# Optimization experiments

Measured on AMD Instinct MI355X. Metric: run time of the kernel, lower is better.

The kernel has to match this reference:

```python
import jax, jax.numpy as jnp
import numpy as np

B, L, H = 4, 512, 768
S, R = 100, 100          # num spans, num relations
E = 25                   # size embedding dim
MAXLEN = 100             # max entity length (size embedding vocab)
NE, NR = 10, 6           # entity / relation type counts
NEG = jnp.float32(-1e20)


def _span_masks(key, batch, n, seqlen, max_len):
    k1, k2 = jax.random.split(key)
    starts = jax.random.randint(k1, (batch, n), 0, seqlen - max_len)
    lens = jax.random.randint(k2, (batch, n), 1, max_len)
    pos = jnp.arange(seqlen)
    m = (pos[None, None, :] >= starts[..., None]) & (pos[None, None, :] < (starts + lens)[..., None])
    return m.astype(jnp.int32)  # (batch, n, seqlen), contiguous 0/1 spans


def setup_inputs() -> dict:
    key = jax.random.key(0)
    ks = jax.random.split(key, 8)
    hidden_states = jax.random.normal(ks[0], (B, L, H), dtype=jnp.float32)
    entity_masks = _span_masks(ks[1], B, S, L, 20)            # span len < MAXLEN
    relation_context_masks = _span_masks(ks[2], B, R, L, 50)  # context len < MAXLEN
    relations = jax.random.randint(ks[3], (B, R, 2), 0, S)
    size_emb = jax.random.normal(ks[4], (MAXLEN, E), dtype=jnp.float32) * 0.02
    w_span = jax.random.normal(ks[5], (E + H, NE), dtype=jnp.float32) * 0.02
    b_span = jnp.zeros((NE,), dtype=jnp.float32)
    w_rel = jax.random.normal(ks[6], (2 * E + 3 * H, NR), dtype=jnp.float32) * 0.02
    b_rel = jnp.zeros((NR,), dtype=jnp.float32)
    return {
        'hidden_states': hidden_states,
        'entity_masks': entity_masks,
        'relations': relations,
        'relation_context_masks': relation_context_masks,
        'size_emb': size_emb,
        'w_span': w_span,
        'b_span': b_span,
        'w_rel': w_rel,
        'b_rel': b_rel,
    }


def _masked_max(hidden, masks):
    # hidden: (B, L, H); masks: (B, N, L) 0/1 -> (B, N, H) max over masked positions
    # Matches torch: h.unsqueeze(1)*m then masked_fill(m==0, -1e20), max over L
    masked = jnp.where(masks[..., None] != 0, hidden[:, None, :, :], NEG)
    return jnp.max(masked, axis=-2)


def reference(hidden_states, entity_masks, relations, relation_context_masks,
              size_emb, w_span, b_span, w_rel, b_rel):
    # entity sizes -> size embedding lookup
    entity_sizes = size_emb[entity_masks.sum(-1)]                     # (B, S, E)

    # entity span max-pool + classify
    entities = _masked_max(hidden_states, entity_masks)               # (B, S, H)
    entity_reprs = jnp.concatenate([entities, entity_sizes], axis=-1)
    entity_logits = entity_reprs @ w_span + b_span                    # (B, S, NE)

    # relation context max-pool
    rel_ctx = _masked_max(hidden_states, relation_context_masks)      # (B, R, H)

    # gather entity pairs
    b, r = relations.shape[:2]
    rel_flat = relations.reshape(b, -1)                               # (B, 2R)
    pairs = jnp.take_along_axis(entities, rel_flat[:, :, None], axis=1).reshape(b, r, -1)
    pair_sizes = jnp.take_along_axis(entity_sizes, rel_flat[:, :, None], axis=1).reshape(b, r, -1)

    rel_reprs = jnp.concatenate([rel_ctx, pairs, pair_sizes], axis=-1)
    relation_logits = rel_reprs @ w_rel + b_rel                       # (B, R, NR)
    return entity_logits, relation_logits
```

## Files before the change

### kernel.cpp

```cpp
#include <hip/hip_runtime.h>

#define B 4
#define L 512
#define H 768
#define S 100
#define R 100
#define E 25
#define NE 10
#define NR 6
#define NEGF (-1e20f)
#define TPB 192

__device__ __forceinline__ float4 fmax4(float4 a, float4 b) {
    return make_float4(fmaxf(a.x, b.x), fmaxf(a.y, b.y),
                       fmaxf(a.z, b.z), fmaxf(a.w, b.w));
}

__device__ __forceinline__ void mask_stats(const int* __restrict__ mrow,
                                           int t, int wave, int lane,
                                           int* sc, int* sm, int& n, int& start)
{
    int4 m = make_int4(0, 0, 0, 0);
    if (t < L / 4) m = reinterpret_cast<const int4*>(mrow)[t];
    const unsigned long long b0 = __ballot(m.x != 0);
    const unsigned long long b1 = __ballot(m.y != 0);
    const unsigned long long b2 = __ballot(m.z != 0);
    const unsigned long long b3 = __ballot(m.w != 0);
    if (lane == 0 && wave < 2) {
        const int c = __popcll(b0) + __popcll(b1) + __popcll(b2) + __popcll(b3);
        int mn = L;
        if (b3) mn = min(mn, 4 * __builtin_ctzll(b3) + 3);
        if (b2) mn = min(mn, 4 * __builtin_ctzll(b2) + 2);
        if (b1) mn = min(mn, 4 * __builtin_ctzll(b1) + 1);
        if (b0) mn = min(mn, 4 * __builtin_ctzll(b0));
        sc[wave] = c;
        sm[wave] = (mn < L) ? (256 * wave + mn) : L;
    }
    __syncthreads();
    n = sc[0] + sc[1];
    start = min(sm[0], sm[1]);
}

__device__ __forceinline__ float4 span_pool4(const float* __restrict__ hb,
                                             int start, int n, int t)
{
    const int st = H / 4;
    const float4* base = reinterpret_cast<const float4*>(hb) + (size_t)start * st + t;
    float4 a0 = make_float4(NEGF, NEGF, NEGF, NEGF);
    float4 a1 = a0, a2 = a0, a3 = a0, a4 = a0, a5 = a0, a6 = a0, a7 = a0;
    const int last = n - 1;
    for (int i = 0; i < n; i += 8) {
        const float4 v0 = base[(size_t)min(i + 0, last) * st];
        const float4 v1 = base[(size_t)min(i + 1, last) * st];
        const float4 v2 = base[(size_t)min(i + 2, last) * st];
        const float4 v3 = base[(size_t)min(i + 3, last) * st];
        const float4 v4 = base[(size_t)min(i + 4, last) * st];
        const float4 v5 = base[(size_t)min(i + 5, last) * st];
        const float4 v6 = base[(size_t)min(i + 6, last) * st];
        const float4 v7 = base[(size_t)min(i + 7, last) * st];
        a0 = fmax4(a0, v0); a1 = fmax4(a1, v1);
        a2 = fmax4(a2, v2); a3 = fmax4(a3, v3);
        a4 = fmax4(a4, v4); a5 = fmax4(a5, v5);
        a6 = fmax4(a6, v6); a7 = fmax4(a7, v7);
    }
    return fmax4(fmax4(fmax4(a0, a1), fmax4(a2, a3)),
                 fmax4(fmax4(a4, a5), fmax4(a6, a7)));
}

template <int NO>
__device__ __forceinline__ void block_reduce_store(float* p, int t, int wave, int lane,
                                                   float (*sred)[NO],
                                                   const float* __restrict__ bias,
                                                   float* __restrict__ outrow)
{
    #pragma unroll
    for (int o = 0; o < NO; ++o) {
        float v = p[o];
        for (int off = 32; off > 0; off >>= 1) v += __shfl_down(v, off, 64);
        p[o] = v;
    }
    if (lane == 0) {
        #pragma unroll
        for (int o = 0; o < NO; ++o) sred[wave][o] = p[o];
    }
    __syncthreads();
    if (t < NO) outrow[t] = sred[0][t] + sred[1][t] + sred[2][t] + bias[t];
}

__global__ __launch_bounds__(TPB) void pool_kernel(
    const float* __restrict__ hidden,
    const int*   __restrict__ emask,
    const int*   __restrict__ cmask,
    const float* __restrict__ size_emb,
    const float* __restrict__ w_span,
    const float* __restrict__ b_span,
    float* __restrict__ entities,
    int*   __restrict__ n_ent,
    float* __restrict__ rel_ctx,
    float* __restrict__ ent_logits)
{
    const int idx  = blockIdx.x;
    const int b    = idx / (S + R);
    const int j    = idx % (S + R);
    const int t    = threadIdx.x;
    const int wave = t >> 6;
    const int lane = t & 63;

    __shared__ int   sc[2], sm[2];
    __shared__ float sred[3][NE];

    const float* hb = hidden + (size_t)b * L * H;
    const int* mrow = (j < S) ? (emask + (size_t)(b * S + j) * L)
                              : (cmask + (size_t)(b * R + (j - S)) * L);
    int n, start;
    mask_stats(mrow, t, wave, lane, sc, sm, n, start);

    const float4 mv = span_pool4(hb, start, n, t);

    if (j >= S) {
        reinterpret_cast<float4*>(rel_ctx + (size_t)(b * R + (j - S)) * H)[t] = mv;
        return;
    }

    reinterpret_cast<float4*>(entities + (size_t)(b * S + j) * H)[t] = mv;
    if (t == 0) n_ent[b * S + j] = n;

    float p[NE];
    const float* w0 = w_span + (size_t)(4 * t) * NE;
    #pragma unroll
    for (int o = 0; o < NE; ++o)
        p[o] = mv.x * w0[o] + mv.y * w0[NE + o] + mv.z * w0[2 * NE + o] + mv.w * w0[3 * NE + o];
    if (t < E) {
        const float sz = size_emb[(size_t)n * E + t];
        #pragma unroll
        for (int o = 0; o < NE; ++o) p[o] += sz * w_span[(size_t)(H + t) * NE + o];
    }
    block_reduce_store<NE>(p, t, wave, lane, sred, b_span,
                           ent_logits + (size_t)(b * S + j) * NE);
}

__global__ __launch_bounds__(TPB) void rel_kernel(
    const float* __restrict__ entities,
    const int*   __restrict__ n_ent,
    const float* __restrict__ rel_ctx,
    const int*   __restrict__ relations,
    const float* __restrict__ size_emb,
    const float* __restrict__ w_rel,
    const float* __restrict__ b_rel,
    float* __restrict__ rel_logits)
{
    const int idx  = blockIdx.x;
    const int b    = idx / R;
    const int r    = idx % R;
    const int t    = threadIdx.x;
    const int wave = t >> 6;
    const int lane = t & 63;

    const int head = relations[(size_t)(b * R + r) * 2 + 0];
    const int tail = relations[(size_t)(b * R + r) * 2 + 1];

    const float4 c4 = reinterpret_cast<const float4*>(rel_ctx  + (size_t)(b * R + r)    * H)[t];
    const float4 h4 = reinterpret_cast<const float4*>(entities + (size_t)(b * S + head) * H)[t];
    const float4 t4 = reinterpret_cast<const float4*>(entities + (size_t)(b * S + tail) * H)[t];

    float p[NR];
    const float* wc = w_rel + (size_t)(4 * t) * NR;
    const float* wh = w_rel + (size_t)(H + 4 * t) * NR;
    const float* wt = w_rel + (size_t)(2 * H + 4 * t) * NR;
    #pragma unroll
    for (int o = 0; o < NR; ++o)
        p[o] = c4.x * wc[o] + c4.y * wc[NR + o] + c4.z * wc[2 * NR + o] + c4.w * wc[3 * NR + o]
             + h4.x * wh[o] + h4.y * wh[NR + o] + h4.z * wh[2 * NR + o] + h4.w * wh[3 * NR + o]
             + t4.x * wt[o] + t4.y * wt[NR + o] + t4.z * wt[2 * NR + o] + t4.w * wt[3 * NR + o];

    if (t < E) {
        const float sz = size_emb[(size_t)n_ent[b * S + head] * E + t];
        #pragma unroll
        for (int o = 0; o < NR; ++o) p[o] += sz * w_rel[(size_t)(3 * H + t) * NR + o];
    } else if (t >= 64 && t < 64 + E) {
        const int e = t - 64;
        const float sz = size_emb[(size_t)n_ent[b * S + tail] * E + e];
        #pragma unroll
        for (int o = 0; o < NR; ++o) p[o] += sz * w_rel[(size_t)(3 * H + E + e) * NR + o];
    }

    __shared__ float sred[3][NR];
    block_reduce_store<NR>(p, t, wave, lane, sred, b_rel,
                           rel_logits + (size_t)(b * R + r) * NR);
}

extern "C" void kernel_launch(void* const* d_in, const int* in_sizes, int n_in,
                              void* d_out, int out_size, void* d_ws, size_t ws_size,
                              hipStream_t stream) {
    const float* hidden    = (const float*)d_in[0];
    const int*   emask     = (const int*)  d_in[1];
    const int*   relations = (const int*)  d_in[2];
    const int*   cmask     = (const int*)  d_in[3];
    const float* size_emb  = (const float*)d_in[4];
    const float* w_span    = (const float*)d_in[5];
    const float* b_span    = (const float*)d_in[6];
    const float* w_rel     = (const float*)d_in[7];
    const float* b_rel     = (const float*)d_in[8];

    float* out        = (float*)d_out;
    float* ent_logits = out;
    float* rel_logits = out + B * S * NE;

    float* ws       = (float*)d_ws;
    float* entities = ws;
    float* rel_ctx  = entities + (size_t)B * S * H;
    int*   n_ent    = (int*)(rel_ctx + (size_t)B * R * H);

    pool_kernel<<<B * (S + R), TPB, 0, stream>>>(
        hidden, emask, cmask, size_emb, w_span, b_span,
        entities, n_ent, rel_ctx, ent_logits);

    rel_kernel<<<B * R, TPB, 0, stream>>>(
        entities, n_ent, rel_ctx, relations, size_emb, w_rel, b_rel, rel_logits);
}
```

Before: 84.79 us.

## Project entities to relation logits before gathering, replacing full-vector gather kernel

Uses the linearity of the relation classifier: each entity's pooled vector and size embedding are projected onto the head and tail halves of w_rel inside the pooling kernel, and each context vector is projected onto its part of w_rel there too. A small combine kernel then gathers and adds those 6-wide projections per relation. This removes writing and re-reading the full 768-wide entity and context vectors through the workspace, and replaces the second block-per-relation kernel with a cheap elementwise one. In exchange, the entity blocks do more reductions (22 outputs instead of 10), and floating-point summation order changes.

```diff
diff --git a/kernel.cpp b/kernel.cpp
--- a/kernel.cpp
+++ b/kernel.cpp
@@ -10,6 +10,7 @@
 #define NR 6
 #define NEGF (-1e20f)
 #define TPB 192
+#define NPROJ (NE + 2*NR)
 
 __device__ __forceinline__ float4 fmax4(float4 a, float4 b) {
     return make_float4(fmaxf(a.x, b.x), fmaxf(a.y, b.y),
@@ -68,23 +69,18 @@
 }
 
 template <int NO>
-__device__ __forceinline__ void block_reduce_store(float* p, int t, int wave, int lane,
-                                                   float (*sred)[NO],
-                                                   const float* __restrict__ bias,
-                                                   float* __restrict__ outrow)
+__device__ __forceinline__ float block_reduce(const float* p, int t, int wave, int lane,
+                                              float sred[3][NPROJ])
 {
     #pragma unroll
     for (int o = 0; o < NO; ++o) {
         float v = p[o];
+        #pragma unroll
         for (int off = 32; off > 0; off >>= 1) v += __shfl_down(v, off, 64);
-        p[o] = v;
-    }
-    if (lane == 0) {
-        #pragma unroll
-        for (int o = 0; o < NO; ++o) sred[wave][o] = p[o];
+        if (lane == 0) sred[wave][o] = v;
     }
     __syncthreads();
-    if (t < NO) outrow[t] = sred[0][t] + sred[1][t] + sred[2][t] + bias[t];
+    return (t < NO) ? (sred[0][t] + sred[1][t] + sred[2][t]) : 0.0f;
 }
 
 __global__ __launch_bounds__(TPB) void pool_kernel(
@@ -94,9 +90,10 @@
     const float* __restrict__ size_emb,
     const float* __restrict__ w_span,
     const float* __restrict__ b_span,
-    float* __restrict__ entities,
-    int*   __restrict__ n_ent,
-    float* __restrict__ rel_ctx,
+    const float* __restrict__ w_rel,
+    const float* __restrict__ b_rel,
+    float* __restrict__ ent_proj,
+    float* __restrict__ ctx_proj,
     float* __restrict__ ent_logits)
 {
     const int idx  = blockIdx.x;
@@ -107,7 +104,7 @@
     const int lane = t & 63;
 
     __shared__ int   sc[2], sm[2];
-    __shared__ float sred[3][NE];
+    __shared__ float sred[3][NPROJ];
 
     const float* hb = hidden + (size_t)b * L * H;
     const int* mrow = (j < S) ? (emask + (size_t)(b * S + j) * L)
@@ -118,75 +115,67 @@
     const float4 mv = span_pool4(hb, start, n, t);
 
     if (j >= S) {
-        reinterpret_cast<float4*>(rel_ctx + (size_t)(b * R + (j - S)) * H)[t] = mv;
+        float p[NR];
+        const float* wc = w_rel + (size_t)(4 * t) * NR;
+        #pragma unroll
+        for (int o = 0; o < NR; ++o)
+            p[o] = mv.x * wc[o] + mv.y * wc[NR + o]
+                 + mv.z * wc[2 * NR + o] + mv.w * wc[3 * NR + o];
+        const float r = block_reduce<NR>(p, t, wave, lane, sred);
+        if (t < NR)
+            ctx_proj[(size_t)(b * R + (j - S)) * NR + t] = r + b_rel[t];
         return;
     }
 
-    reinterpret_cast<float4*>(entities + (size_t)(b * S + j) * H)[t] = mv;
-    if (t == 0) n_ent[b * S + j] = n;
-
-    float p[NE];
+    float p[NPROJ];
     const float* w0 = w_span + (size_t)(4 * t) * NE;
+    const float* wh = w_rel  + (size_t)(H + 4 * t) * NR;
+    const float* wt = w_rel  + (size_t)(2 * H + 4 * t) * NR;
     #pragma unroll
     for (int o = 0; o < NE; ++o)
-        p[o] = mv.x * w0[o] + mv.y * w0[NE + o] + mv.z * w0[2 * NE + o] + mv.w * w0[3 * NE + o];
+        p[o] = mv.x * w0[o] + mv.y * w0[NE + o]
+             + mv.z * w0[2 * NE + o] + mv.w * w0[3 * NE + o];
+    #pragma unroll
+    for (int o = 0; o < NR; ++o) {
+        p[NE + o]      = mv.x * wh[o] + mv.y * wh[NR + o]
+                       + mv.z * wh[2 * NR + o] + mv.w * wh[3 * NR + o];
+        p[NE + NR + o] = mv.x * wt[o] + mv.y * wt[NR + o]
+                       + mv.z * wt[2 * NR + o] + mv.w * wt[3 * NR + o];
+    }
     if (t < E) {
         const float sz = size_emb[(size_t)n * E + t];
         #pragma unroll
-        for (int o = 0; o < NE; ++o) p[o] += sz * w_span[(size_t)(H + t) * NE + o];
-    }
-    block_reduce_store<NE>(p, t, wave, lane, sred, b_span,
-                           ent_logits + (size_t)(b * S + j) * NE);
-}
-
-__global__ __launch_bounds__(TPB) void rel_kernel(
-    const float* __restrict__ entities,
-    const int*   __restrict__ n_ent,
-    const float* __restrict__ rel_ctx,
+        for (int o = 0; o < NE; ++o)
+            p[o] += sz * w_span[(size_t)(H + t) * NE + o];
+        #pragma unroll
+        for (int o = 0; o < NR; ++o) {
+            p[NE + o]      += sz * w_rel[(size_t)(3 * H + t) * NR + o];
+            p[NE + NR + o] += sz * w_rel[(size_t)(3 * H + E + t) * NR + o];
+        }
+    }
+    const float r = block_reduce<NPROJ>(p, t, wave, lane, sred);
+    if (t < NE)
+        ent_logits[(size_t)(b * S + j) * NE + t] = r + b_span[t];
+    else if (t < NPROJ)
+        ent_proj[(size_t)(b * S + j) * (2 * NR) + (t - NE)] = r;
+}
+
+__global__ __launch_bounds__(256) void combine_kernel(
+    const float* __restrict__ ent_proj,
+    const float* __restrict__ ctx_proj,
     const int*   __restrict__ relations,
-    const float* __restrict__ size_emb,
-    const float* __restrict__ w_rel,
-    const float* __restrict__ b_rel,
     float* __restrict__ rel_logits)
 {
-    const int idx  = blockIdx.x;
-    const int b    = idx / R;
-    const int r    = idx % R;
-    const int t    = threadIdx.x;
-    const int wave = t >> 6;
-    const int lane = t & 63;
-
-    const int head = relations[(size_t)(b * R + r) * 2 + 0];
-    const int tail = relations[(size_t)(b * R + r) * 2 + 1];
-
-    const float4 c4 = reinterpret_cast<const float4*>(rel_ctx  + (size_t)(b * R + r)    * H)[t];
-    const float4 h4 = reinterpret_cast<const float4*>(entities + (size_t)(b * S + head) * H)[t];
-    const float4 t4 = reinterpret_cast<const float4*>(entities + (size_t)(b * S + tail) * H)[t];
-
-    float p[NR];
-    const float* wc = w_rel + (size_t)(4 * t) * NR;
-    const float* wh = w_rel + (size_t)(H + 4 * t) * NR;
-    const float* wt = w_rel + (size_t)(2 * H + 4 * t) * NR;
-    #pragma unroll
-    for (int o = 0; o < NR; ++o)
-        p[o] = c4.x * wc[o] + c4.y * wc[NR + o] + c4.z * wc[2 * NR + o] + c4.w * wc[3 * NR + o]
-             + h4.x * wh[o] + h4.y * wh[NR + o] + h4.z * wh[2 * NR + o] + h4.w * wh[3 * NR + o]
-             + t4.x * wt[o] + t4.y * wt[NR + o] + t4.z * wt[2 * NR + o] + t4.w * wt[3 * NR + o];
-
-    if (t < E) {
-        const float sz = size_emb[(size_t)n_ent[b * S + head] * E + t];
-        #pragma unroll
-        for (int o = 0; o < NR; ++o) p[o] += sz * w_rel[(size_t)(3 * H + t) * NR + o];
-    } else if (t >= 64 && t < 64 + E) {
-        const int e = t - 64;
-        const float sz = size_emb[(size_t)n_ent[b * S + tail] * E + e];
-        #pragma unroll
-        for (int o = 0; o < NR; ++o) p[o] += sz * w_rel[(size_t)(3 * H + E + e) * NR + o];
-    }
-
-    __shared__ float sred[3][NR];
-    block_reduce_store<NR>(p, t, wave, lane, sred, b_rel,
-                           rel_logits + (size_t)(b * R + r) * NR);
+    const int g = blockIdx.x * 256 + threadIdx.x;
+    if (g >= B * R * NR) return;
+    const int o  = g % NR;
+    const int br = g / NR;
+    const int b  = br / R;
+    const int head = relations[(size_t)br * 2 + 0];
+    const int tail = relations[(size_t)br * 2 + 1];
+    rel_logits[g] = ctx_proj[g]
+                  + ent_proj[(size_t)(b * S + head) * (2 * NR) + o]
+                  + ent_proj[(size_t)(b * S + tail) * (2 * NR) + NR + o];
 }
 
 extern "C" void kernel_launch(void* const* d_in, const int* in_sizes, int n_in,
@@ -207,14 +196,13 @@
     float* rel_logits = out + B * S * NE;
 
     float* ws       = (float*)d_ws;
-    float* entities = ws;
-    float* rel_ctx  = entities + (size_t)B * S * H;
-    int*   n_ent    = (int*)(rel_ctx + (size_t)B * R * H);
+    float* ent_proj = ws;
+    float* ctx_proj = ent_proj + (size_t)B * S * 2 * NR;
 
     pool_kernel<<<B * (S + R), TPB, 0, stream>>>(
-        hidden, emask, cmask, size_emb, w_span, b_span,
-        entities, n_ent, rel_ctx, ent_logits);
-
-    rel_kernel<<<B * R, TPB, 0, stream>>>(
-        entities, n_ent, rel_ctx, relations, size_emb, w_rel, b_rel, rel_logits);
-}
+        hidden, emask, cmask, size_emb, w_span, b_span, w_rel, b_rel,
+        ent_proj, ctx_proj, ent_logits);
+
+    combine_kernel<<<(B * R * NR + 255) / 256, 256, 0, stream>>>(
+        ent_proj, ctx_proj, relations, rel_logits);
+}
```

After: 87.79 us. 1.04x slower.
